# Performance work log

Hardware: AMD Instinct MI355X
Metric: run time of the kernel (lower is better)

## Reference

```python
import jax, jax.numpy as jnp
from jax import lax
import numpy as np


def conv2d(x, w, b, stride=1, pad=0):
    # x: [B,C,H,W], w: [O,I,kh,kw]
    y = lax.conv_general_dilated(
        x, w, (stride, stride), [(pad, pad), (pad, pad)],
        dimension_numbers=("NCHW", "OIHW", "NCHW"))
    return y + b[None, :, None, None]


def setup_inputs() -> dict:
    key = jax.random.key(0)
    ks = jax.random.split(key, 9)
    B, C, Ci, H, W = 1, 64, 32, 96, 96
    sc3 = 1.0 / np.sqrt(C * 9)   # fan-in scale for 3x3 convs
    sc1 = 1.0 / np.sqrt(C)       # fan-in scale for 1x1 convs
    scw = 1.0 / np.sqrt(Ci)
    return {
        "x":    jax.random.normal(ks[0], (B, C, H, W), jnp.float32),
        "d1_w": jax.random.normal(ks[1], (C, C, 3, 3), jnp.float32) * sc3,
        "d1_b": jnp.zeros((C,), jnp.float32),
        "d2_w": jax.random.normal(ks[2], (C, C, 3, 3), jnp.float32) * sc3,
        "d2_b": jnp.zeros((C,), jnp.float32),
        "d3_w": jax.random.normal(ks[3], (C, C, 3, 3), jnp.float32) * sc3,
        "d3_b": jnp.zeros((C,), jnp.float32),
        "g_w":  jax.random.normal(ks[4], (Ci, C, 1, 1), jnp.float32) * sc1,
        "g_b":  jnp.zeros((Ci,), jnp.float32),
        "th_w": jax.random.normal(ks[5], (Ci, C, 1, 1), jnp.float32) * sc1,
        "th_b": jnp.zeros((Ci,), jnp.float32),
        "ph_w": jax.random.normal(ks[6], (Ci, C, 1, 1), jnp.float32) * sc1,
        "ph_b": jnp.zeros((Ci,), jnp.float32),
        "W_w":  jax.random.normal(ks[7], (C, Ci, 1, 1), jnp.float32) * scw,
        "W_b":  jnp.zeros((C,), jnp.float32),
    }


def reference(x, d1_w, d1_b, d2_w, d2_b, d3_w, d3_b,
              g_w, g_b, th_w, th_b, ph_w, ph_b, W_w, W_b):
    lrelu = lambda v: jnp.where(v >= 0, v, 0.2 * v)
    y = lrelu(conv2d(x, d1_w, d1_b, stride=2, pad=1))
    y = lrelu(conv2d(y, d2_w, d2_b, stride=2, pad=1))
    y = conv2d(y, d3_w, d3_b, stride=2, pad=1)
    y = jax.image.resize(y, x.shape, method="bilinear")  # align_corners=False semantics
    x = jax.nn.sigmoid(y) * x
    # --- non-local block ---
    B, C, H, W = x.shape
    Ci = g_w.shape[0]
    gx = conv2d(x, g_w, g_b).reshape(B, Ci, -1)    # [B,Ci,N]
    tx = conv2d(x, th_w, th_b).reshape(B, Ci, -1)  # [B,Ci,N]
    px = conv2d(x, ph_w, ph_b).reshape(B, Ci, -1)  # [B,Ci,N]
    # f[b,n,m] = sum_c theta[b,n,c] * phi[b,c,m]  (N x N scores, no scaling)
    f = jnp.einsum("bcn,bcm->bnm", tx, px)
    f = jax.nn.softmax(f, axis=1)  # unconventional: softmax over FIRST token axis
    # y[b,c,n] = sum_m f[b,n,m] * g[b,c,m]
    y2 = jnp.einsum("bnm,bcm->bcn", f, gx).reshape(B, Ci, H, W)
    return conv2d(y2, W_w, W_b) + x
```

## Files before the change

### kernel.cpp

```cpp
#include <hip/hip_runtime.h>
#include <math.h>

#define NTOK 9216
#define CIN  32
#define CC   64
#define NCH1 24
#define NT1S 24
#define NCH2 16
#define MS2  18
#define MCH2 576
#define LOG2E 1.4426950408889634f
#define C1INIT (-17.312340490667560f)
#define C2INIT (-9.3123404906675595f)

typedef _Float16 half8 __attribute__((ext_vector_type(8)));
typedef float    f32x4 __attribute__((ext_vector_type(4)));

static __device__ __forceinline__ float fexp2(float x) {
#if __has_builtin(__builtin_amdgcn_exp2f)
    return __builtin_amdgcn_exp2f(x);
#else
    return exp2f(x);
#endif
}

__global__ void conv3x3_quad96(const float* __restrict__ in, const float* __restrict__ w,
                               float* __restrict__ outp) {
    const int t = threadIdx.x;
    const int q = t % 12, ohl = t / 12;
    const int oh = blockIdx.x * 16 + ohl;
    const int oc = blockIdx.y, grp = blockIdx.z;
    const int ci0 = grp * 4;
    float a0 = 0.f, a1 = 0.f, a2 = 0.f, a3 = 0.f;
    const int iwl = 8 * q - 1;
    #pragma unroll
    for (int ci = 0; ci < 4; ++ci) {
        const float* ip = in + (ci0 + ci) * 9216;
        const float* wp = w + oc * CC * 9 + (ci0 + ci) * 9;
        #pragma unroll
        for (int kh = 0; kh < 3; ++kh) {
            int ih = oh * 2 - 1 + kh;
            if (ih < 0) continue;
            const float* rp = ip + ih * 96;
            float ls = (q > 0) ? rp[iwl] : 0.f;
            float4 fa = *(const float4*)(rp + 8 * q);
            float4 fb = *(const float4*)(rp + 8 * q + 4);
            float w0 = wp[kh * 3], w1 = wp[kh * 3 + 1], w2 = wp[kh * 3 + 2];
            a0 = fmaf(ls,   w0, fmaf(fa.x, w1, fmaf(fa.y, w2, a0)));
            a1 = fmaf(fa.y, w0, fmaf(fa.z, w1, fmaf(fa.w, w2, a1)));
            a2 = fmaf(fa.w, w0, fmaf(fb.x, w1, fmaf(fb.y, w2, a2)));
            a3 = fmaf(fb.y, w0, fmaf(fb.z, w1, fmaf(fb.w, w2, a3)));
        }
    }
    float4 r = make_float4(a0, a1, a2, a3);
    *(float4*)(outp + grp * (CC * 2304) + oc * 2304 + oh * 48 + 4 * q) = r;
}

template<int HIN, int HOUT, int CIG>
__global__ void conv3x3_part(const float* __restrict__ in, const float* __restrict__ w,
                             float* __restrict__ outp) {
    const int p = blockIdx.x * blockDim.x + threadIdx.x;
    if (p >= HOUT * HOUT) return;
    const int oc = blockIdx.y, grp = blockIdx.z;
    const int oh = p / HOUT, ow = p % HOUT;
    const int ci0 = grp * CIG;
    float acc = 0.f;
    #pragma unroll
    for (int ci = 0; ci < CIG; ++ci) {
        const float* ip = in + (ci0 + ci) * HIN * HIN;
        const float* wp = w + oc * CC * 9 + (ci0 + ci) * 9;
        #pragma unroll
        for (int kh = 0; kh < 3; ++kh) {
            int ih = oh * 2 - 1 + kh;
            bool okh = (unsigned)ih < (unsigned)HIN;
            #pragma unroll
            for (int kw = 0; kw < 3; ++kw) {
                int iw = ow * 2 - 1 + kw;
                float v = (okh && (unsigned)iw < (unsigned)HIN) ? ip[ih * HIN + iw] : 0.f;
                acc = fmaf(v, wp[kh * 3 + kw], acc);
            }
        }
    }
    outp[grp * (CC * HOUT * HOUT) + oc * HOUT * HOUT + p] = acc;
}

template<int NG, int HW, int LRELU>
__global__ void conv_merge4(const float* __restrict__ parts, const float* __restrict__ b,
                            float* __restrict__ out) {
    int i4 = blockIdx.x * 256 + threadIdx.x;
    int oc = (i4 * 4) / HW;
    float bb = b[oc];
    float4 acc = make_float4(bb, bb, bb, bb);
    #pragma unroll
    for (int g = 0; g < NG; ++g) {
        float4 p = *(const float4*)(parts + g * (CC * HW) + i4 * 4);
        acc.x += p.x; acc.y += p.y; acc.z += p.z; acc.w += p.w;
    }
    if (LRELU) {
        acc.x = acc.x >= 0.f ? acc.x : 0.2f * acc.x;
        acc.y = acc.y >= 0.f ? acc.y : 0.2f * acc.y;
        acc.z = acc.z >= 0.f ? acc.z : 0.2f * acc.z;
        acc.w = acc.w >= 0.f ? acc.w : 0.2f * acc.w;
    }
    *(float4*)(out + i4 * 4) = acc;
}

static __device__ __forceinline__ float gate_val(const float* y3c, int n) {
    int h = n / 96, wc = n % 96;
    float fh = (h + 0.5f) * 0.125f - 0.5f;
    float fw = (wc + 0.5f) * 0.125f - 0.5f;
    int h0 = (int)floorf(fh); float ah = fh - (float)h0;
    int w0 = (int)floorf(fw); float aw = fw - (float)w0;
    int h0c = min(max(h0, 0), 11), h1c = min(max(h0 + 1, 0), 11);
    int w0c = min(max(w0, 0), 11), w1c = min(max(w0 + 1, 0), 11);
    float v = (1.f - ah) * ((1.f - aw) * y3c[h0c * 12 + w0c] + aw * y3c[h0c * 12 + w1c])
            +         ah * ((1.f - aw) * y3c[h1c * 12 + w0c] + aw * y3c[h1c * 12 + w1c]);
    return 1.f / (1.f + __expf(-v));
}

__global__ void gate_fused(const float* __restrict__ x, const float* __restrict__ cp3,
                           const float* __restrict__ d3b, float* __restrict__ xg) {
    __shared__ float y3c[144];
    const int b = blockIdx.x, t = threadIdx.x;
    const int c = b / 36;
    if (t < 144) {
        float acc = d3b[c];
        #pragma unroll
        for (int g = 0; g < 16; ++g)
            acc += cp3[g * (CC * 144) + c * 144 + t];
        y3c[t] = acc;
    }
    __syncthreads();
    int idx = b * 256 + t;
    int n = idx % 9216;
    float sg = gate_val(y3c, n);
    xg[idx] = sg * x[idx];
}

__global__ void conv1x1_frag(const float* __restrict__ xg,
                             const float* __restrict__ gw, const float* __restrict__ gb,
                             const float* __restrict__ thw, const float* __restrict__ thb,
                             const float* __restrict__ phw, const float* __restrict__ phb,
                             _Float16* __restrict__ txF, _Float16* __restrict__ pxF,
                             _Float16* __restrict__ gxF) {
    int ci = blockIdx.y;
    int n = blockIdx.x * 256 + threadIdx.x;
    float ag = gb[ci], at = thb[ci], ap = phb[ci];
    #pragma unroll 8
    for (int c = 0; c < CC; ++c) {
        float v = xg[c * NTOK + n];
        ag = fmaf(gw[ci * CC + c],  v, ag);
        at = fmaf(thw[ci * CC + c], v, at);
        ap = fmaf(phw[ci * CC + c], v, ap);
    }
    int addr_ab = (n >> 4) * 512 + (((n & 15) | (((ci & 15) >> 2) << 4)) * 8)
                + (((ci >> 4) << 2) | (ci & 3));
    txF[addr_ab] = (_Float16)(at * LOG2E);
    pxF[addr_ab] = (_Float16)ap;
    int addr_g = ((n >> 5) * 2 + (ci >> 4)) * 512
               + (((ci & 15) | (((n & 15) >> 2) << 4)) * 8)
               + ((((n >> 4) & 1) << 2) | (n & 3));
    gxF[addr_g] = (_Float16)ag;
}

__global__ __launch_bounds__(256) void phase1(const _Float16* __restrict__ txF,
                                              const _Float16* __restrict__ pxF,
                                              float* __restrict__ Dp) {
    int w = threadIdx.x >> 6, l = threadIdx.x & 63;
    int mtile0 = (blockIdx.x * 4 + w) * 4;
    half8 pf[4];
    #pragma unroll
    for (int j = 0; j < 4; ++j)
        pf[j] = *(const half8*)(pxF + (mtile0 + j) * 512 + l * 8);
    f32x4 cini = {C1INIT, C1INIT, C1INIT, C1INIT};
    float dsum[4][4] = {};
    int nt0 = blockIdx.y * NT1S;
    #pragma unroll 2
    for (int i = 0; i < NT1S; ++i) {
        half8 tf = *(const half8*)(txF + (nt0 + i) * 512 + l * 8);
        #pragma unroll
        for (int j = 0; j < 4; ++j) {
            f32x4 s = __builtin_amdgcn_mfma_f32_16x16x32_f16(pf[j], tf, cini, 0, 0, 0);
            #pragma unroll
            for (int r = 0; r < 4; ++r)
                dsum[j][r] += fexp2(s[r]);
        }
    }
    #pragma unroll
    for (int off = 1; off < 16; off <<= 1)
        #pragma unroll
        for (int j = 0; j < 4; ++j)
            #pragma unroll
            for (int r = 0; r < 4; ++r)
                dsum[j][r] += __shfl_xor(dsum[j][r], off);
    if ((l & 15) == 0) {
        #pragma unroll
        for (int j = 0; j < 4; ++j) {
            int m = (mtile0 + j) * 16 + (l >> 4) * 4;
            #pragma unroll
            for (int r = 0; r < 4; ++r)
                Dp[blockIdx.y * NTOK + m + r] = dsum[j][r];
        }
    }
}

__global__ __launch_bounds__(256) void phase2(const _Float16* __restrict__ txF,
                                              const _Float16* __restrict__ pxF,
                                              const _Float16* __restrict__ gxF,
                                              const float* __restrict__ Dp,
                                              float* __restrict__ y2p) {
    __shared__ float l2D[MCH2];
    int mbase = blockIdx.y * MCH2;
    for (int i = threadIdx.x; i < MCH2; i += 256) {
        float D = 0.f;
        #pragma unroll
        for (int ch = 0; ch < NCH1; ++ch) D += Dp[ch * NTOK + mbase + i];
        l2D[i] = __log2f(D);
    }
    __syncthreads();
    int w = threadIdx.x >> 6, l = threadIdx.x & 63;
    int ntile0 = (blockIdx.x * 4 + w) * 4;
    half8 tf[4];
    #pragma unroll
    for (int j = 0; j < 4; ++j)
        tf[j] = *(const half8*)(txF + (ntile0 + j) * 512 + l * 8);
    int khi = (l >> 4) * 4;
    f32x4 zero = {0.f, 0.f, 0.f, 0.f};
    f32x4 c2v = {C2INIT, C2INIT, C2INIT, C2INIT};
    f32x4 acc[4][2];
    #pragma unroll
    for (int j = 0; j < 4; ++j) { acc[j][0] = zero; acc[j][1] = zero; }
    #pragma unroll 2
    for (int ms = 0; ms < MS2; ++ms) {
        int m0 = mbase + ms * 32;
        int mloc = ms * 32;
        int mt16 = m0 >> 4;
        half8 pf0 = *(const half8*)(pxF + mt16 * 512 + l * 8);
        half8 pf1 = *(const half8*)(pxF + (mt16 + 1) * 512 + l * 8);
        f32x4 l2a = *(const f32x4*)&l2D[mloc + khi];
        f32x4 l2b = *(const f32x4*)&l2D[mloc + 16 + khi];
        f32x4 cini0 = c2v - l2a;
        f32x4 cini1 = c2v - l2b;
        int gt = (m0 >> 5) * 2;
        half8 gf0 = *(const half8*)(gxF + gt * 512 + l * 8);
        half8 gf1 = *(const half8*)(gxF + (gt + 1) * 512 + l * 8);
        #pragma unroll
        for (int j = 0; j < 4; ++j) {
            f32x4 s0 = __builtin_amdgcn_mfma_f32_16x16x32_f16(pf0, tf[j], cini0, 0, 0, 0);
            f32x4 s1 = __builtin_amdgcn_mfma_f32_16x16x32_f16(pf1, tf[j], cini1, 0, 0, 0);
            half8 ff;
            #pragma unroll
            for (int r = 0; r < 4; ++r) {
                ff[r]     = (_Float16)fexp2(s0[r]);
                ff[4 + r] = (_Float16)fexp2(s1[r]);
            }
            acc[j][0] = __builtin_amdgcn_mfma_f32_16x16x32_f16(ff, gf0, acc[j][0], 0, 0, 0);
            acc[j][1] = __builtin_amdgcn_mfma_f32_16x16x32_f16(ff, gf1, acc[j][1], 0, 0, 0);
        }
    }
    float* base = y2p + blockIdx.y * (CIN * NTOK);
    #pragma unroll
    for (int j = 0; j < 4; ++j) {
        int n = (ntile0 + j) * 16 + khi;
        #pragma unroll
        for (int r = 0; r < 4; ++r) {
            base[(l & 15) * NTOK + n + r]        = acc[j][0][r] * 0.00390625f;
            base[(16 + (l & 15)) * NTOK + n + r] = acc[j][1][r] * 0.00390625f;
        }
    }
}

__global__ void mergeY2(const float* __restrict__ y2p, float* __restrict__ att) {
    int i4 = blockIdx.x * 256 + threadIdx.x;
    float4 s = make_float4(0.f, 0.f, 0.f, 0.f);
    #pragma unroll
    for (int ch = 0; ch < NCH2; ++ch) {
        float4 p = *(const float4*)(y2p + ch * (CIN * NTOK) + i4 * 4);
        s.x += p.x; s.y += p.y; s.z += p.z; s.w += p.w;
    }
    *(float4*)(att + i4 * 4) = s;
}

__global__ void final_conv(const float* __restrict__ att, const float* __restrict__ Ww,
                           const float* __restrict__ Wb, const float* __restrict__ xg,
                           float* __restrict__ out) {
    int co = blockIdx.y;
    int n = blockIdx.x * 256 + threadIdx.x;
    float acc = Wb[co];
    #pragma unroll
    for (int ci = 0; ci < CIN; ++ci)
        acc = fmaf(Ww[co * CIN + ci], att[ci * NTOK + n], acc);
    out[co * NTOK + n] = acc + xg[co * NTOK + n];
}

extern "C" void kernel_launch(void* const* d_in, const int* in_sizes, int n_in,
                              void* d_out, int out_size, void* d_ws, size_t ws_size,
                              hipStream_t stream) {
    const float* x   = (const float*)d_in[0];
    const float* d1w = (const float*)d_in[1];  const float* d1b = (const float*)d_in[2];
    const float* d2w = (const float*)d_in[3];  const float* d2b = (const float*)d_in[4];
    const float* d3w = (const float*)d_in[5];  const float* d3b = (const float*)d_in[6];
    const float* gw  = (const float*)d_in[7];  const float* gb  = (const float*)d_in[8];
    const float* thw = (const float*)d_in[9];  const float* thb = (const float*)d_in[10];
    const float* phw = (const float*)d_in[11]; const float* phb = (const float*)d_in[12];
    const float* Ww  = (const float*)d_in[13]; const float* Wb  = (const float*)d_in[14];
    float* out = (float*)d_out;

    float* W    = (float*)d_ws;
    float* xg   = W;
    float* y1   = W + 589824;
    float* y2c  = W + 737280;
    float* Dp   = W + 774144;
    float* att  = W + 995328;
    float* y2p  = W + 1290240;
    _Float16* txF = (_Float16*)(W + 6008832);
    _Float16* pxF = (_Float16*)(W + 6156288);
    _Float16* gxF = (_Float16*)(W + 6303744);

    float* cp1 = y2p;
    float* cp2 = y2p + 2359296;
    float* cp3 = y2p + 2949120;

    conv3x3_quad96<<<dim3(3, CC, 16), 192, 0, stream>>>(x, d1w, cp1);
    conv_merge4<16, 2304, 1><<<144, 256, 0, stream>>>(cp1, d1b, y1);
    conv3x3_part<48, 24, 4><<<dim3(3, CC, 16), 192, 0, stream>>>(y1, d2w, cp2);
    conv_merge4<16, 576, 1><<<36, 256, 0, stream>>>(cp2, d2b, y2c);
    conv3x3_part<24, 12, 4><<<dim3(1, CC, 16), 192, 0, stream>>>(y2c, d3w, cp3);
    gate_fused<<<2304, 256, 0, stream>>>(x, cp3, d3b, xg);

    conv1x1_frag<<<dim3(36, CIN), 256, 0, stream>>>(xg, gw, gb, thw, thb, phw, phb,
                                                    txF, pxF, gxF);

    phase1<<<dim3(36, NCH1), 256, 0, stream>>>(txF, pxF, Dp);
    phase2<<<dim3(36, NCH2), 256, 0, stream>>>(txF, pxF, gxF, Dp, y2p);
    mergeY2<<<288, 256, 0, stream>>>(y2p, att);

    final_conv<<<dim3(36, CC), 256, 0, stream>>>(att, Ww, Wb, xg, out);
}
```

Baseline: 121.6 us.

## Stage first conv inputs and weights in LDS; store phase2 partials in fp16

The first stride-2 3x3 conv now stages the three input rows and all 64 output-channel weights for one output row and four input channels in shared memory. Each thread then computes a 4x4 register tile of pixels and output channels, so global input reads are no longer repeated for every output channel. Separately, the phase2 partial attention outputs are written and merged as fp16 instead of fp32, halving that intermediate traffic at some cost in precision. The workspace layout is reorganized so the conv partials and the fp16 buffer no longer alias.

```diff
diff --git a/kernel.cpp b/kernel.cpp
--- a/kernel.cpp
+++ b/kernel.cpp
@@ -14,6 +14,7 @@
 #define C2INIT (-9.3123404906675595f)
 
 typedef _Float16 half8 __attribute__((ext_vector_type(8)));
+typedef _Float16 half4v __attribute__((ext_vector_type(4)));
 typedef float    f32x4 __attribute__((ext_vector_type(4)));
 
 static __device__ __forceinline__ float fexp2(float x) {
@@ -24,36 +25,58 @@
 #endif
 }
 
-__global__ void conv3x3_quad96(const float* __restrict__ in, const float* __restrict__ w,
-                               float* __restrict__ outp) {
+__global__ __launch_bounds__(192) void conv3x3_lds96(const float* __restrict__ in,
+                                                     const float* __restrict__ w,
+                                                     float* __restrict__ outp) {
+    __shared__ float li[4][3][100];
+    __shared__ float lw[4][9][64];
     const int t = threadIdx.x;
-    const int q = t % 12, ohl = t / 12;
-    const int oh = blockIdx.x * 16 + ohl;
-    const int oc = blockIdx.y, grp = blockIdx.z;
+    const int oh = blockIdx.x, grp = blockIdx.y;
     const int ci0 = grp * 4;
-    float a0 = 0.f, a1 = 0.f, a2 = 0.f, a3 = 0.f;
-    const int iwl = 8 * q - 1;
+    for (int idx = t; idx < 4 * 3 * 97; idx += 192) {
+        int ci = idx / (3 * 97), rem = idx % (3 * 97);
+        int kh = rem / 97, col = rem % 97;
+        int ih = 2 * oh - 1 + kh, iw = col - 1;
+        float v = 0.f;
+        if (ih >= 0 && iw >= 0) v = in[(ci0 + ci) * 9216 + ih * 96 + iw];
+        li[ci][kh][col] = v;
+    }
+    for (int idx = t; idx < 4 * 9 * 64; idx += 192) {
+        int oc = idx / 36, r = idx % 36;
+        int ci = r / 9, k = r % 9;
+        lw[ci][k][oc] = w[oc * 576 + (ci0 + ci) * 9 + k];
+    }
+    __syncthreads();
+    const int oc0 = (t & 15) * 4;
+    const int ow0 = (t >> 4) * 4;
+    float acc[4][4] = {};
     #pragma unroll
     for (int ci = 0; ci < 4; ++ci) {
-        const float* ip = in + (ci0 + ci) * 9216;
-        const float* wp = w + oc * CC * 9 + (ci0 + ci) * 9;
+        float wr[9][4];
+        #pragma unroll
+        for (int k = 0; k < 9; ++k)
+            *(float4*)wr[k] = *(const float4*)&lw[ci][k][oc0];
         #pragma unroll
         for (int kh = 0; kh < 3; ++kh) {
-            int ih = oh * 2 - 1 + kh;
-            if (ih < 0) continue;
-            const float* rp = ip + ih * 96;
-            float ls = (q > 0) ? rp[iwl] : 0.f;
-            float4 fa = *(const float4*)(rp + 8 * q);
-            float4 fb = *(const float4*)(rp + 8 * q + 4);
-            float w0 = wp[kh * 3], w1 = wp[kh * 3 + 1], w2 = wp[kh * 3 + 2];
-            a0 = fmaf(ls,   w0, fmaf(fa.x, w1, fmaf(fa.y, w2, a0)));
-            a1 = fmaf(fa.y, w0, fmaf(fa.z, w1, fmaf(fa.w, w2, a1)));
-            a2 = fmaf(fa.w, w0, fmaf(fb.x, w1, fmaf(fb.y, w2, a2)));
-            a3 = fmaf(fb.y, w0, fmaf(fb.z, w1, fmaf(fb.w, w2, a3)));
-        }
-    }
-    float4 r = make_float4(a0, a1, a2, a3);
-    *(float4*)(outp + grp * (CC * 2304) + oc * 2304 + oh * 48 + 4 * q) = r;
+            float v[9];
+            #pragma unroll
+            for (int j = 0; j < 9; ++j) v[j] = li[ci][kh][2 * ow0 + j];
+            #pragma unroll
+            for (int px = 0; px < 4; ++px)
+                #pragma unroll
+                for (int kw = 0; kw < 3; ++kw) {
+                    float xv = v[2 * px + kw];
+                    #pragma unroll
+                    for (int o = 0; o < 4; ++o)
+                        acc[px][o] = fmaf(xv, wr[kh * 3 + kw][o], acc[px][o]);
+                }
+        }
+    }
+    float* op = outp + grp * (CC * 2304) + oh * 48 + ow0;
+    #pragma unroll
+    for (int o = 0; o < 4; ++o)
+        *(float4*)(op + (oc0 + o) * 2304) =
+            make_float4(acc[0][o], acc[1][o], acc[2][o], acc[3][o]);
 }
 
 template<int HIN, int HOUT, int CIG>
@@ -208,7 +231,7 @@
                                               const _Float16* __restrict__ pxF,
                                               const _Float16* __restrict__ gxF,
                                               const float* __restrict__ Dp,
-                                              float* __restrict__ y2p) {
+                                              _Float16* __restrict__ y2p) {
     __shared__ float l2D[MCH2];
     int mbase = blockIdx.y * MCH2;
     for (int i = threadIdx.x; i < MCH2; i += 256) {
@@ -258,25 +281,28 @@
             acc[j][1] = __builtin_amdgcn_mfma_f32_16x16x32_f16(ff, gf1, acc[j][1], 0, 0, 0);
         }
     }
-    float* base = y2p + blockIdx.y * (CIN * NTOK);
+    _Float16* base = y2p + blockIdx.y * (CIN * NTOK);
     #pragma unroll
     for (int j = 0; j < 4; ++j) {
         int n = (ntile0 + j) * 16 + khi;
+        half4v v0, v1;
         #pragma unroll
         for (int r = 0; r < 4; ++r) {
-            base[(l & 15) * NTOK + n + r]        = acc[j][0][r] * 0.00390625f;
-            base[(16 + (l & 15)) * NTOK + n + r] = acc[j][1][r] * 0.00390625f;
-        }
-    }
-}
-
-__global__ void mergeY2(const float* __restrict__ y2p, float* __restrict__ att) {
+            v0[r] = (_Float16)(acc[j][0][r] * 0.00390625f);
+            v1[r] = (_Float16)(acc[j][1][r] * 0.00390625f);
+        }
+        *(half4v*)(base + (l & 15) * NTOK + n)        = v0;
+        *(half4v*)(base + (16 + (l & 15)) * NTOK + n) = v1;
+    }
+}
+
+__global__ void mergeY2(const _Float16* __restrict__ y2p, float* __restrict__ att) {
     int i4 = blockIdx.x * 256 + threadIdx.x;
     float4 s = make_float4(0.f, 0.f, 0.f, 0.f);
     #pragma unroll
     for (int ch = 0; ch < NCH2; ++ch) {
-        float4 p = *(const float4*)(y2p + ch * (CIN * NTOK) + i4 * 4);
-        s.x += p.x; s.y += p.y; s.z += p.z; s.w += p.w;
+        half4v p = *(const half4v*)(y2p + ch * (CIN * NTOK) + i4 * 4);
+        s.x += (float)p[0]; s.y += (float)p[1]; s.z += (float)p[2]; s.w += (float)p[3];
     }
     *(float4*)(att + i4 * 4) = s;
 }
@@ -312,16 +338,15 @@
     float* y2c  = W + 737280;
     float* Dp   = W + 774144;
     float* att  = W + 995328;
-    float* y2p  = W + 1290240;
-    _Float16* txF = (_Float16*)(W + 6008832);
-    _Float16* pxF = (_Float16*)(W + 6156288);
-    _Float16* gxF = (_Float16*)(W + 6303744);
-
-    float* cp1 = y2p;
-    float* cp2 = y2p + 2359296;
-    float* cp3 = y2p + 2949120;
-
-    conv3x3_quad96<<<dim3(3, CC, 16), 192, 0, stream>>>(x, d1w, cp1);
+    float* cp1  = W + 1290240;
+    float* cp2  = W + 3649536;
+    float* cp3  = W + 4239360;
+    _Float16* txF  = (_Float16*)(W + 4386816);
+    _Float16* pxF  = (_Float16*)(W + 4534272);
+    _Float16* gxF  = (_Float16*)(W + 4681728);
+    _Float16* y2pH = (_Float16*)(W + 4829184);
+
+    conv3x3_lds96<<<dim3(48, 16), 192, 0, stream>>>(x, d1w, cp1);
     conv_merge4<16, 2304, 1><<<144, 256, 0, stream>>>(cp1, d1b, y1);
     conv3x3_part<48, 24, 4><<<dim3(3, CC, 16), 192, 0, stream>>>(y1, d2w, cp2);
     conv_merge4<16, 576, 1><<<36, 256, 0, stream>>>(cp2, d2b, y2c);
@@ -332,8 +357,8 @@
                                                     txF, pxF, gxF);
 
     phase1<<<dim3(36, NCH1), 256, 0, stream>>>(txF, pxF, Dp);
-    phase2<<<dim3(36, NCH2), 256, 0, stream>>>(txF, pxF, gxF, Dp, y2p);
-    mergeY2<<<288, 256, 0, stream>>>(y2p, att);
+    phase2<<<dim3(36, NCH2), 256, 0, stream>>>(txF, pxF, gxF, Dp, y2pH);
+    mergeY2<<<288, 256, 0, stream>>>(y2pH, att);
 
     final_conv<<<dim3(36, CC), 256, 0, stream>>>(att, Ww, Wb, xg, out);
 }
```

After: 105.9 us. -13.0%, faster.
